# Kernel optimization log

Hardware: AMD Instinct MI355X
Metric: run time of the kernel (lower is better)

The kernel has to match this reference:

```python
import jax, jax.numpy as jnp
import numpy as np

HIDDEN = 1024
EMBED = 1024
SEQ = 512
BATCH = 64


def setup_inputs() -> dict:
    key = jax.random.key(0)
    k1, k2, k3 = jax.random.split(key, 3)
    factor = 1.0 / np.sqrt(HIDDEN)
    embeds = jax.random.normal(k1, (SEQ, BATCH, EMBED), dtype=jnp.float32)
    w = jax.random.uniform(k2, (HIDDEN + EMBED, 4 * HIDDEN), dtype=jnp.float32,
                           minval=-factor, maxval=factor)
    b = jax.random.uniform(k3, (4 * HIDDEN,), dtype=jnp.float32,
                           minval=-factor, maxval=factor)
    # forget-gate bias += 1 (gate order is g, i, f, o)
    b = b.at[2 * HIDDEN:3 * HIDDEN].add(1.0)
    return {"embeds": embeds, "w": w, "b": b}


def reference(embeds, w, b):
    T, B, E = embeds.shape
    H = w.shape[1] // 4

    def step(carry, x_t):
        h, c = carry
        data = jnp.concatenate([h, x_t], axis=-1)          # [B, H+E]
        big = data @ w + b                                  # [B, 4H]
        g, i, f, o = jnp.split(big, 4, axis=1)
        g = jnp.tanh(g)
        i = jax.nn.sigmoid(i)
        f = jax.nn.sigmoid(f)
        o = jax.nn.sigmoid(o)
        c_new = g * i + c * f
        h_new = jnp.tanh(c_new) * o
        return (h_new, c_new), h_new

    h0 = jnp.zeros((B, H), dtype=embeds.dtype)
    c0 = jnp.zeros((B, H), dtype=embeds.dtype)
    _, out = jax.lax.scan(step, (h0, c0), embeds)           # out: [T, B, H]
    return out
```

## Files before the change

kernel.cpp:

```cpp
#include <hip/hip_runtime.h>
#include <stdint.h>


#define TSTEPS 512
#define NBATCH 64
#define NHID   1024
#define NWG2   64
#define FLAGSTRIDE 32
#define AGENT  __HIP_MEMORY_SCOPE_AGENT

typedef __attribute__((ext_vector_type(8))) short bf16x8;
typedef __attribute__((ext_vector_type(4))) float f32x4;
typedef __attribute__((ext_vector_type(4))) int   i32x4;
typedef __attribute__((ext_vector_type(4))) float fl4;

__device__ __forceinline__ uint16_t f2bf(float f){
  uint32_t u = __float_as_uint(f);
  u += 0x7fffu + ((u >> 16) & 1u);
  return (uint16_t)(u >> 16);
}
__device__ __forceinline__ float bf2f(uint16_t b){
  return __uint_as_float(((uint32_t)b) << 16);
}
__device__ __forceinline__ float sigm(float x){ return 1.0f/(1.0f + __expf(-x)); }
__device__ __forceinline__ float tanhfast(float x){ return 1.0f - 2.0f/(__expf(2.0f*x) + 1.0f); }
__device__ __forceinline__ bf16x8 as_bf(i32x4 v){
  union { i32x4 i; bf16x8 b; } u; u.i = v; return u.b;
}

__global__ void k0a_cvt(const float* __restrict__ in, uint16_t* __restrict__ outp, int n8){
  int stride = gridDim.x * blockDim.x;
  for (int i = blockIdx.x * blockDim.x + threadIdx.x; i < n8; i += stride){
    const fl4* p = (const fl4*)(in + (size_t)i * 8);
    fl4 v0 = p[0], v1 = p[1];
    union { uint16_t u[8]; i32x4 v; } r;
    r.u[0]=f2bf(v0.x); r.u[1]=f2bf(v0.y); r.u[2]=f2bf(v0.z); r.u[3]=f2bf(v0.w);
    r.u[4]=f2bf(v1.x); r.u[5]=f2bf(v1.y); r.u[6]=f2bf(v1.z); r.u[7]=f2bf(v1.w);
    *(i32x4*)(outp + (size_t)i * 8) = r.v;
  }
}

__global__ void k0b_trans(const float* __restrict__ w, uint16_t* __restrict__ wT){
  __shared__ float tile[64 * 65];
  int k0 = blockIdx.x * 64;
  int n0 = blockIdx.y * 64;
  int tid = threadIdx.x;
  int r  = tid >> 2;
  int cq = (tid & 3) * 16;
#pragma unroll
  for (int i = 0; i < 4; ++i){
    fl4 v = *(const fl4*)(w + (size_t)(k0 + r) * 4096 + n0 + cq + i * 4);
    tile[r*65 + cq + i*4 + 0] = v.x;
    tile[r*65 + cq + i*4 + 1] = v.y;
    tile[r*65 + cq + i*4 + 2] = v.z;
    tile[r*65 + cq + i*4 + 3] = v.w;
  }
  __syncthreads();
  union { uint16_t u[8]; i32x4 v; } a, b;
#pragma unroll
  for (int i = 0; i < 8; ++i) a.u[i] = f2bf(tile[(cq + i) * 65 + r]);
#pragma unroll
  for (int i = 0; i < 8; ++i) b.u[i] = f2bf(tile[(cq + 8 + i) * 65 + r]);
  *(i32x4*)(wT + (size_t)(n0 + r) * 2048 + k0 + cq)     = a.v;
  *(i32x4*)(wT + (size_t)(n0 + r) * 2048 + k0 + cq + 8) = b.v;
}

__launch_bounds__(256, 2)
__global__ void k1_xw(const uint16_t* __restrict__ ebf, const uint16_t* __restrict__ wT,
                      const float* __restrict__ bias, uint16_t* __restrict__ xw){
  __shared__ char sm[32768];
  char* As = sm;
  char* Bs = sm + 16384;
  int bid = blockIdx.x;
  int nt = bid & 31, mt = bid >> 5;
  int m0 = mt * 128, n0 = nt * 128;
  int tid = threadIdx.x;
  int lane = tid & 63, wid = tid >> 6;
  int wr = wid >> 1, wc = wid & 1;

  f32x4 zero = {0.f, 0.f, 0.f, 0.f};
  f32x4 acc[4][4];
#pragma unroll
  for (int mi = 0; mi < 4; ++mi)
#pragma unroll
    for (int ni = 0; ni < 4; ++ni) acc[mi][ni] = zero;

  for (int kt = 0; kt < 16; ++kt){
    __syncthreads();
#pragma unroll
    for (int i = 0; i < 4; ++i){
      int L = i * 256 + tid;
      int row = L >> 3, c = L & 7;
      i32x4 va = *(const i32x4*)(ebf + (size_t)(m0 + row) * 1024 + kt * 64 + c * 8);
      *(i32x4*)(As + row * 128 + ((c ^ (row & 7)) * 16)) = va;
      i32x4 vb = *(const i32x4*)(wT + (size_t)(n0 + row) * 2048 + 1024 + kt * 64 + c * 8);
      *(i32x4*)(Bs + row * 128 + ((c ^ (row & 7)) * 16)) = vb;
    }
    __syncthreads();
#pragma unroll
    for (int kk = 0; kk < 2; ++kk){
      bf16x8 a[4], b[4];
      int ci = kk * 4 + (lane >> 4);
#pragma unroll
      for (int mi = 0; mi < 4; ++mi){
        int rl = wr * 64 + mi * 16 + (lane & 15);
        a[mi] = *(const bf16x8*)(As + rl * 128 + ((ci ^ (rl & 7)) * 16));
      }
#pragma unroll
      for (int ni = 0; ni < 4; ++ni){
        int sl = wc * 64 + ni * 16 + (lane & 15);
        b[ni] = *(const bf16x8*)(Bs + sl * 128 + ((ci ^ (sl & 7)) * 16));
      }
#pragma unroll
      for (int mi = 0; mi < 4; ++mi)
#pragma unroll
        for (int ni = 0; ni < 4; ++ni)
          acc[mi][ni] = __builtin_amdgcn_mfma_f32_16x16x32_bf16(a[mi], b[ni], acc[mi][ni], 0, 0, 0);
    }
  }
  float bcol[4];
#pragma unroll
  for (int ni = 0; ni < 4; ++ni) bcol[ni] = bias[n0 + wc * 64 + ni * 16 + (lane & 15)];
#pragma unroll
  for (int mi = 0; mi < 4; ++mi)
#pragma unroll
    for (int ni = 0; ni < 4; ++ni)
#pragma unroll
      for (int jj = 0; jj < 4; ++jj){
        int rg = m0 + wr * 64 + mi * 16 + (lane >> 4) * 4 + jj;
        int cg = n0 + wc * 64 + ni * 16 + (lane & 15);
        __builtin_nontemporal_store(f2bf(acc[mi][ni][jj] + bcol[ni]),
                                    &xw[(size_t)rg * 4096 + cg]);
      }
}

#define LDA(k, OFF) asm volatile("global_load_dwordx4 %0, %1, off offset:" #OFF \
                                 : "=v"(ap[k]) : "v"(aB) : "memory")
#define WAITV(N) do { asm volatile("s_waitcnt vmcnt(" #N ")" ::: "memory"); \
                      __builtin_amdgcn_sched_barrier(0); } while(0)
#define GBLK(K0) \
  _Pragma("unroll") \
  for (int kc = K0; kc < K0 + 8; ++kc){ \
    bf16x8 a = as_bf(ap[kc]); \
    _Pragma("unroll") \
    for (int g = 0; g < 4; ++g){ \
      bf16x8 b = *(const bf16x8*)(WP + ((kc * 4 + g) << 10) + (lane << 4)); \
      acc[g] = __builtin_amdgcn_mfma_f32_16x16x32_bf16(a, b, acc[g], 0, 0, 0); \
    } \
  }

__launch_bounds__(256, 1)
__global__ void k2_rec(const uint16_t* __restrict__ xw, const uint16_t* __restrict__ wT,
                       uint16_t* __restrict__ hbuf, int* __restrict__ flags,
                       float* __restrict__ outp){
  extern __shared__ char sm[];
  char* WP = sm;

  int tid  = threadIdx.x;
  int lane = tid & 63;
  int w    = tid >> 6;
  int wg = blockIdx.x;
  int j0 = wg * 16;

#pragma unroll
  for (int i = 0; i < 32; ++i){
    int L = i * 256 + tid;
    int kc = L >> 8;
    int g  = (L >> 6) & 3;
    int l6 = L & 63;
    int q_ = (l6 >> 4) & 3;
    int rr_ = l6 & 15;
    i32x4 v = *(const i32x4*)(wT + (size_t)(g * 1024 + j0 + rr_) * 2048 + kc * 32 + q_ * 8);
    *(i32x4*)(WP + (size_t)L * 16) = v;
  }
  __syncthreads();

  const int r0 = w * 16;
  const int q  = lane >> 4;
  const int rr = lane & 15;

  float creg[4] = {0.f, 0.f, 0.f, 0.f};

  uint16_t xc[4][4], xn[4][4];
  {
    const uint16_t* xp0 = xw + j0 + rr;
    const uint16_t* xp1 = xw + (size_t)1 * (64 * 4096) + j0 + rr;
#pragma unroll
    for (int g = 0; g < 4; ++g)
#pragma unroll
      for (int p = 0; p < 4; ++p){
        xc[g][p] = xp0[(size_t)(r0 + q * 4 + p) * 4096 + g * 1024];
        xn[g][p] = xp1[(size_t)(r0 + q * 4 + p) * 4096 + g * 1024];
      }
  }

  for (int t = 0; t < TSTEPS; ++t){
    if (t > 0){
      int fi = (lane * 4 + w) * FLAGSTRIDE;
      while (true){
        int v = __hip_atomic_load(&flags[fi], __ATOMIC_RELAXED, AGENT);
        if (__all(v >= t)) break;
        __builtin_amdgcn_s_sleep(1);
      }
    }

    const uint16_t* hsrc = hbuf + (size_t)t * (NBATCH * NHID);
    const uint16_t* aB = hsrc + (size_t)(r0 + rr) * 1024 + q * 8;
    i32x4 ap[32];
    LDA(0,0);     LDA(1,64);    LDA(2,128);   LDA(3,192);
    LDA(4,256);   LDA(5,320);   LDA(6,384);   LDA(7,448);
    LDA(8,512);   LDA(9,576);   LDA(10,640);  LDA(11,704);
    LDA(12,768);  LDA(13,832);  LDA(14,896);  LDA(15,960);
    LDA(16,1024); LDA(17,1088); LDA(18,1152); LDA(19,1216);
    LDA(20,1280); LDA(21,1344); LDA(22,1408); LDA(23,1472);
    LDA(24,1536); LDA(25,1600); LDA(26,1664); LDA(27,1728);
    LDA(28,1792); LDA(29,1856); LDA(30,1920); LDA(31,1984);

    uint16_t xn2[4][4];
    {
      int tn = (t < TSTEPS - 2) ? t + 2 : TSTEPS - 1;
      const uint16_t* xp = xw + (size_t)tn * (64 * 4096) + j0 + rr;
#pragma unroll
      for (int g = 0; g < 4; ++g)
#pragma unroll
        for (int p = 0; p < 4; ++p)
          xn2[g][p] = __builtin_nontemporal_load(
                        &xp[(size_t)(r0 + q * 4 + p) * 4096 + g * 1024]);
    }

    f32x4 acc[4];
#pragma unroll
    for (int g = 0; g < 4; ++g) acc[g] = (f32x4){0.f, 0.f, 0.f, 0.f};

    WAITV(40); GBLK(0);
    WAITV(32); GBLK(8);
    WAITV(24); GBLK(16);
    WAITV(16); GBLK(24);

    uint16_t* hdst = hbuf + (size_t)(t + 1) * (NBATCH * NHID);
#pragma unroll
    for (int p = 0; p < 4; ++p){
      float G = acc[0][p] + bf2f(xc[0][p]);
      float I = acc[1][p] + bf2f(xc[1][p]);
      float F = acc[2][p] + bf2f(xc[2][p]);
      float O = acc[3][p] + bf2f(xc[3][p]);
      G = tanhfast(G); I = sigm(I); F = sigm(F); O = sigm(O);
      float c = G * I + creg[p] * F;
      creg[p] = c;
      float h = tanhfast(c) * O;
      __hip_atomic_store(hdst + (size_t)(r0 + q * 4 + p) * 1024 + j0 + rr,
                         f2bf(h), __ATOMIC_RELAXED, AGENT);
    }

    asm volatile("s_waitcnt vmcnt(0)" ::: "memory");
    if (lane == 0)
      __hip_atomic_store(&flags[(wg * 4 + w) * FLAGSTRIDE], t + 1, __ATOMIC_RELAXED, AGENT);

#pragma unroll
    for (int g = 0; g < 4; ++g)
#pragma unroll
      for (int p = 0; p < 4; ++p){
        xc[g][p] = xn[g][p];
        xn[g][p] = xn2[g][p];
      }
  }
}

__global__ void k3_out(const uint16_t* __restrict__ hb, float* __restrict__ outp, int n8){
  int stride = gridDim.x * blockDim.x;
  for (int i = blockIdx.x * blockDim.x + threadIdx.x; i < n8; i += stride){
    i32x4 v = *(const i32x4*)(hb + (size_t)(NBATCH * NHID) + (size_t)i * 8);
    const uint16_t* u = (const uint16_t*)&v;
    fl4 o0, o1;
    o0.x = bf2f(u[0]); o0.y = bf2f(u[1]); o0.z = bf2f(u[2]); o0.w = bf2f(u[3]);
    o1.x = bf2f(u[4]); o1.y = bf2f(u[5]); o1.z = bf2f(u[6]); o1.w = bf2f(u[7]);
    __builtin_nontemporal_store(o0, (fl4*)(outp + (size_t)i * 8));
    __builtin_nontemporal_store(o1, (fl4*)(outp + (size_t)i * 8 + 4));
  }
}

extern "C" void kernel_launch(void* const* d_in, const int* in_sizes, int n_in,
                              void* d_out, int out_size, void* d_ws, size_t ws_size,
                              hipStream_t stream){
  const float* embeds = (const float*)d_in[0];
  const float* w      = (const float*)d_in[1];
  const float* bias   = (const float*)d_in[2];
  float* outp = (float*)d_out;
  char* ws = (char*)d_ws;

  const size_t o_ebf = 0;
  const size_t o_wT  = o_ebf + (size_t)32768 * 1024 * 2;
  const size_t o_xw  = o_wT  + (size_t)4096 * 2048 * 2;
  const size_t o_hb  = o_xw  + (size_t)32768 * 4096 * 2;
  const size_t o_fl  = o_hb  + (size_t)513 * 64 * 1024 * 2;

  uint16_t* ebf  = (uint16_t*)(ws + o_ebf);
  uint16_t* wT   = (uint16_t*)(ws + o_wT);
  uint16_t* xw   = (uint16_t*)(ws + o_xw);
  uint16_t* hbuf = (uint16_t*)(ws + o_hb);
  int*      flags= (int*)(ws + o_fl);

  hipMemsetAsync(ws + o_hb, 0, (size_t)64 * 1024 * 2, stream);
  hipMemsetAsync(ws + o_fl, 0, 256 * FLAGSTRIDE * sizeof(int), stream);

  k0a_cvt<<<2048, 256, 0, stream>>>(embeds, ebf, (512 * 64 * 1024) / 8);
  k0b_trans<<<dim3(32, 64), 256, 0, stream>>>(w, wT);
  k1_xw<<<8192, 256, 0, stream>>>(ebf, wT, bias, xw);

  (void)hipFuncSetAttribute((const void*)k2_rec,
                            hipFuncAttributeMaxDynamicSharedMemorySize, 131072);
  k2_rec<<<NWG2, 256, 131072, stream>>>(xw, wT, hbuf, flags, outp);

  k3_out<<<2048, 256, 0, stream>>>(hbuf, outp, (512 * 64 * 1024) / 8);
}
```

Baseline: 4.474 ms.

## Split recurrent step wait into half-K chunks with rotated chunk order

Each workgroup now waits only on the producers of the first half of the hidden dimension (rotated by workgroup index), starts the MFMA on those two K chunks, and only then waits on the remaining producers before loading and computing the other half. Flags are re-laid out per wave and producer with a tighter stride, and polling and posting use explicit sc0/sc1 loads and stores. The aim is to overlap partial matmul work with the global barrier latency and to spread the workgroups' access order. In exchange, the reduced flag stride puts several flags in one cache line, which may add contention, and there is now a second poll loop per step.

```diff
diff --git a/kernel.cpp b/kernel.cpp
--- a/kernel.cpp
+++ b/kernel.cpp
@@ -6,7 +6,7 @@
 #define NBATCH 64
 #define NHID   1024
 #define NWG2   64
-#define FLAGSTRIDE 32
+#define FLAGSTRIDE 4
 #define AGENT  __HIP_MEMORY_SCOPE_AGENT
 
 typedef __attribute__((ext_vector_type(8))) short bf16x8;
@@ -134,20 +134,25 @@
       }
 }
 
-#define LDA(k, OFF) asm volatile("global_load_dwordx4 %0, %1, off offset:" #OFF \
-                                 : "=v"(ap[k]) : "v"(aB) : "memory")
+#define LDA(k, BASE, OFF) asm volatile("global_load_dwordx4 %0, %1, off offset:" #OFF \
+                                 : "=v"(ap[k]) : "v"(BASE) : "memory")
+#define LDCHUNK(B, BASE) \
+  LDA((B)*8+0, BASE, 0);   LDA((B)*8+1, BASE, 64);  LDA((B)*8+2, BASE, 128); LDA((B)*8+3, BASE, 192); \
+  LDA((B)*8+4, BASE, 256); LDA((B)*8+5, BASE, 320); LDA((B)*8+6, BASE, 384); LDA((B)*8+7, BASE, 448)
 #define WAITV(N) do { asm volatile("s_waitcnt vmcnt(" #N ")" ::: "memory"); \
                       __builtin_amdgcn_sched_barrier(0); } while(0)
-#define GBLK(K0) \
+#define GBLKR(B, WPC) \
   _Pragma("unroll") \
-  for (int kc = K0; kc < K0 + 8; ++kc){ \
-    bf16x8 a = as_bf(ap[kc]); \
+  for (int i = 0; i < 8; ++i){ \
+    bf16x8 a = as_bf(ap[(B) * 8 + i]); \
     _Pragma("unroll") \
     for (int g = 0; g < 4; ++g){ \
-      bf16x8 b = *(const bf16x8*)(WP + ((kc * 4 + g) << 10) + (lane << 4)); \
+      bf16x8 b = *(const bf16x8*)((WPC) + ((i * 4 + g) << 10) + (lane << 4)); \
       acc[g] = __builtin_amdgcn_mfma_f32_16x16x32_bf16(a, b, acc[g], 0, 0, 0); \
     } \
   }
+#define POLLLD(V, P) asm volatile("global_load_dword %0, %1, off sc0 sc1\n\ts_waitcnt vmcnt(0)" \
+                                  : "=v"(V) : "v"(P) : "memory")
 
 __launch_bounds__(256, 1)
 __global__ void k2_rec(const uint16_t* __restrict__ xw, const uint16_t* __restrict__ wT,
@@ -161,6 +166,7 @@
   int w    = tid >> 6;
   int wg = blockIdx.x;
   int j0 = wg * 16;
+  int rot = wg & 3;
 
 #pragma unroll
   for (int i = 0; i < 32; ++i){
@@ -179,6 +185,19 @@
   const int q  = lane >> 4;
   const int rr = lane & 15;
 
+  const int chk = (rot + (lane >> 4)) & 3;
+  const int* fpoll = flags + (size_t)((w << 6) + (chk << 4) + (lane & 15)) * FLAGSTRIDE;
+  int* fpost = flags + (size_t)((w << 6) + wg) * FLAGSTRIDE;
+
+  char* WPc0 = WP + (((rot + 0) & 3) << 15);
+  char* WPc1 = WP + (((rot + 1) & 3) << 15);
+  char* WPc2 = WP + (((rot + 2) & 3) << 15);
+  char* WPc3 = WP + (((rot + 3) & 3) << 15);
+  const int aOff0 = ((rot + 0) & 3) << 8;
+  const int aOff1 = ((rot + 1) & 3) << 8;
+  const int aOff2 = ((rot + 2) & 3) << 8;
+  const int aOff3 = ((rot + 3) & 3) << 8;
+
   float creg[4] = {0.f, 0.f, 0.f, 0.f};
 
   uint16_t xc[4][4], xn[4][4];
@@ -195,27 +214,44 @@
   }
 
   for (int t = 0; t < TSTEPS; ++t){
+    bool need2 = false;
     if (t > 0){
-      int fi = (lane * 4 + w) * FLAGSTRIDE;
       while (true){
-        int v = __hip_atomic_load(&flags[fi], __ATOMIC_RELAXED, AGENT);
-        if (__all(v >= t)) break;
+        int v; POLLLD(v, fpoll);
+        unsigned long long m = __ballot(v >= t);
+        if ((m & 0xFFFFFFFFull) == 0xFFFFFFFFull){
+          need2 = ((m >> 32) != 0xFFFFFFFFull);
+          break;
+        }
         __builtin_amdgcn_s_sleep(1);
       }
     }
 
     const uint16_t* hsrc = hbuf + (size_t)t * (NBATCH * NHID);
     const uint16_t* aB = hsrc + (size_t)(r0 + rr) * 1024 + q * 8;
+
     i32x4 ap[32];
-    LDA(0,0);     LDA(1,64);    LDA(2,128);   LDA(3,192);
-    LDA(4,256);   LDA(5,320);   LDA(6,384);   LDA(7,448);
-    LDA(8,512);   LDA(9,576);   LDA(10,640);  LDA(11,704);
-    LDA(12,768);  LDA(13,832);  LDA(14,896);  LDA(15,960);
-    LDA(16,1024); LDA(17,1088); LDA(18,1152); LDA(19,1216);
-    LDA(20,1280); LDA(21,1344); LDA(22,1408); LDA(23,1472);
-    LDA(24,1536); LDA(25,1600); LDA(26,1664); LDA(27,1728);
-    LDA(28,1792); LDA(29,1856); LDA(30,1920); LDA(31,1984);
-
+    LDCHUNK(0, aB + aOff0);
+    LDCHUNK(1, aB + aOff1);
+
+    f32x4 acc[4];
+#pragma unroll
+    for (int g = 0; g < 4; ++g) acc[g] = (f32x4){0.f, 0.f, 0.f, 0.f};
+
+    WAITV(8);  GBLKR(0, WPc0);
+    WAITV(0);  GBLKR(1, WPc1);
+
+    if (need2){
+      while (true){
+        int v; POLLLD(v, fpoll);
+        unsigned long long m = __ballot(v >= t);
+        if ((m >> 32) == 0xFFFFFFFFull) break;
+        __builtin_amdgcn_s_sleep(1);
+      }
+    }
+
+    LDCHUNK(2, aB + aOff2);
+    LDCHUNK(3, aB + aOff3);
     uint16_t xn2[4][4];
     {
       int tn = (t < TSTEPS - 2) ? t + 2 : TSTEPS - 1;
@@ -228,14 +264,8 @@
                         &xp[(size_t)(r0 + q * 4 + p) * 4096 + g * 1024]);
     }
 
-    f32x4 acc[4];
-#pragma unroll
-    for (int g = 0; g < 4; ++g) acc[g] = (f32x4){0.f, 0.f, 0.f, 0.f};
-
-    WAITV(40); GBLK(0);
-    WAITV(32); GBLK(8);
-    WAITV(24); GBLK(16);
-    WAITV(16); GBLK(24);
+    WAITV(24); GBLKR(2, WPc2);
+    WAITV(16); GBLKR(3, WPc3);
 
     uint16_t* hdst = hbuf + (size_t)(t + 1) * (NBATCH * NHID);
 #pragma unroll
@@ -253,8 +283,11 @@
     }
 
     asm volatile("s_waitcnt vmcnt(0)" ::: "memory");
-    if (lane == 0)
-      __hip_atomic_store(&flags[(wg * 4 + w) * FLAGSTRIDE], t + 1, __ATOMIC_RELAXED, AGENT);
+    if (lane == 0){
+      int tv = t + 1;
+      asm volatile("global_store_dword %0, %1, off sc0 sc1"
+                   :: "v"(fpost), "v"(tv) : "memory");
+    }
 
 #pragma unroll
     for (int g = 0; g < 4; ++g)
```

New measurement: 3.994 ms. 1.12x faster.
